# Optimization experiments

Measured on AMD Instinct MI355X. Metric: run time of the kernel, lower is better.

The kernel has to match this reference:

```python
import jax, jax.numpy as jnp
import numpy as np

B, L, C = 2, 2048, 1024
H, HD = 16, 64
MAX_SCALE_MUL = float(np.log(100.0))
SCALE = 1.0  # attn_l2_norm=True -> scale is 1


def setup_inputs() -> dict:
    key = jax.random.key(0)
    ks = jax.random.split(key, 6)
    x = jax.random.normal(ks[0], (B, L, C), dtype=jnp.float32)
    attn_bias = jax.random.normal(ks[1], (1, 1, L, L), dtype=jnp.float32)
    w_qkv = jax.random.normal(ks[2], (3 * C, C), dtype=jnp.float32) * (1.0 / np.sqrt(C))
    q_bias = jnp.zeros((C,), dtype=jnp.float32)
    v_bias = jnp.zeros((C,), dtype=jnp.float32)
    scale_mul = jnp.full((1, H, 1, 1), np.log(4.0), dtype=jnp.float32)  # scale_mul_1H11
    w_proj = jax.random.normal(ks[3], (C, C), dtype=jnp.float32) * (1.0 / np.sqrt(C))
    b_proj = jnp.zeros((C,), dtype=jnp.float32)
    return {"x": x, "attn_bias": attn_bias, "w_qkv": w_qkv, "q_bias": q_bias,
            "v_bias": v_bias, "scale_mul": scale_mul, "w_proj": w_proj, "b_proj": b_proj}


def reference(x, attn_bias, w_qkv, q_bias, v_bias, scale_mul, w_proj, b_proj):
    # qkv projection with concatenated bias (q_bias, zeros, v_bias)
    bias = jnp.concatenate([q_bias, jnp.zeros_like(q_bias), v_bias])  # [3C]
    qkv = jnp.einsum('blc,dc->bld', x, w_qkv) + bias                  # [B,L,3C]
    qkv = qkv.reshape(B, L, 3, H, HD).transpose(2, 0, 3, 1, 4)        # [3,B,H,L,HD]
    q, k, v = qkv[0], qkv[1], qkv[2]
    # attn_l2_norm path: L2-normalize q,k; q scaled by exp(clamped scale_mul)
    sm = jnp.exp(jnp.minimum(scale_mul, MAX_SCALE_MUL))               # [1,H,1,1]
    q = q / jnp.linalg.norm(q, axis=-1, keepdims=True) * sm
    k = k / jnp.linalg.norm(k, axis=-1, keepdims=True)
    # slow_attn: scaled scores + bias, softmax, weighted sum
    attn = jnp.einsum('bhld,bhmd->bhlm', q * SCALE, k) + attn_bias    # [B,H,L,L]
    p = jax.nn.softmax(attn, axis=-1)
    oup = jnp.einsum('bhlm,bhmd->bhld', p, v)                         # [B,H,L,HD]
    oup = oup.transpose(0, 2, 1, 3).reshape(B, L, C)
    return jnp.einsum('blc,dc->bld', oup, w_proj) + b_proj
```

## Files before the change

kernel.cpp:

```cpp
#include <hip/hip_runtime.h>
#include <cstdint>
#include <cstddef>
#include <math.h>

typedef __attribute__((ext_vector_type(8))) __bf16 bf16x8;
typedef __attribute__((ext_vector_type(4))) __bf16 bf16x4;
typedef __attribute__((ext_vector_type(4))) float f32x4;

#define AS1 __attribute__((address_space(1)))
#define AS3 __attribute__((address_space(3)))

#define LOG2E 1.4426950408889634f

__device__ __forceinline__ void gld16(void* lds_uniform, const void* gaddr) {
  __builtin_amdgcn_global_load_lds((const AS1 unsigned int*)gaddr,
                                   (AS3 unsigned int*)lds_uniform, 16, 0, 0);
}

__global__ __launch_bounds__(256)
void prep_kernel(const float* __restrict__ x, const float* __restrict__ wqkv,
                 const float* __restrict__ wproj, const float* __restrict__ bias,
                 __bf16* __restrict__ xb, __bf16* __restrict__ wqkvb,
                 __bf16* __restrict__ wprojb, __bf16* __restrict__ btr) {
  __shared__ __bf16 T[32][264];
  const int b = blockIdx.x;
  const int tid = threadIdx.x;
  if (b < 8192) {
    const float* src; __bf16* dst; int off;
    if (b < 4096)      { src = x;     dst = xb;     off = b; }
    else if (b < 7168) { src = wqkv;  dst = wqkvb;  off = b - 4096; }
    else               { src = wproj; dst = wprojb; off = b - 7168; }
    const int i = (off * 256 + tid) * 4;
    const float4 v = *(const float4*)(src + i);
    bf16x4 o;
    o[0] = (__bf16)v.x; o[1] = (__bf16)v.y; o[2] = (__bf16)v.z; o[3] = (__bf16)v.w;
    *(bf16x4*)(dst + i) = o;
    return;
  }
  const int bb = b - 8192;
  const int rb = bb >> 3, cg = bb & 7;
  const float* src = bias + (size_t)(rb * 32) * 2048 + cg * 256;
#pragma unroll
  for (int i = 0; i < 8; ++i) {
    const int u = i * 256 + tid;
    const int r = u >> 6, c4 = (u & 63) * 4;
    const float4 v = *(const float4*)(src + (size_t)r * 2048 + c4);
    T[r][c4 + 0] = (__bf16)(v.x * LOG2E);
    T[r][c4 + 1] = (__bf16)(v.y * LOG2E);
    T[r][c4 + 2] = (__bf16)(v.z * LOG2E);
    T[r][c4 + 3] = (__bf16)(v.w * LOG2E);
  }
  __syncthreads();
  const int ktl = tid >> 6;
  const int lane = tid & 63, g = lane >> 4, c = lane & 15;
  __bf16 outv[32];
#pragma unroll
  for (int v = 0; v < 32; ++v) {
    const int mi = v >> 4, ni = (v >> 2) & 3, j = v & 3;
    outv[v] = T[mi * 16 + g * 4 + j][ktl * 64 + ni * 16 + c];
  }
  __bf16* dst = btr + ((size_t)(rb * 32 + cg * 4 + ktl) * 64 + lane) * 32;
#pragma unroll
  for (int i = 0; i < 4; ++i)
    *(bf16x8*)(dst + i * 8) = *(bf16x8*)(outv + i * 8);
}

__global__ __launch_bounds__(256, 2)
void gemm_qkv_kernel(const __bf16* __restrict__ A, const __bf16* __restrict__ B,
                     const float* __restrict__ q_bias, const float* __restrict__ v_bias,
                     const float* __restrict__ scale_mul,
                     __bf16* __restrict__ qb, __bf16* __restrict__ ktp, __bf16* __restrict__ vb) {
  __shared__ __attribute__((aligned(16))) __bf16 As[128 * 32];
  __shared__ __attribute__((aligned(16))) __bf16 Bs[128 * 32];
  const int tid = threadIdx.x;
  const int w = tid >> 6, lane = tid & 63;
  const int m0 = blockIdx.y * 128, n0 = blockIdx.x * 128;
  const int wm = (w >> 1) * 64, wn = (w & 1) * 64;
  const int c = lane & 15, g = lane >> 4;
  f32x4 acc[4][4];
#pragma unroll
  for (int i = 0; i < 4; ++i)
#pragma unroll
    for (int j = 0; j < 4; ++j) acc[i][j] = (f32x4)(0.0f);

  const int r_row = lane >> 2;
  const int r_col = (lane & 3) * 16;
  const char* Abase = (const char*)A + (size_t)m0 * 2048;
  const char* Bbase = (const char*)B + (size_t)n0 * 2048;

  for (int kt = 0; kt < 1024; kt += 32) {
#pragma unroll
    for (int s = 0; s < 2; ++s) {
      const int R = w * 2 + s;
      const int row = R * 16 + r_row;
      gld16((char*)As + R * 1024, Abase + (size_t)row * 2048 + kt * 2 + r_col);
      gld16((char*)Bs + R * 1024, Bbase + (size_t)row * 2048 + kt * 2 + r_col);
    }
    __syncthreads();
    bf16x8 af[4], bfr[4];
#pragma unroll
    for (int i = 0; i < 4; ++i) {
      af[i]  = *(const bf16x8*)((const char*)As + (wm + i * 16 + c) * 64 + g * 16);
      bfr[i] = *(const bf16x8*)((const char*)Bs + (wn + i * 16 + c) * 64 + g * 16);
    }
#pragma unroll
    for (int ni = 0; ni < 4; ++ni)
#pragma unroll
      for (int mi = 0; mi < 4; ++mi)
        acc[ni][mi] = __builtin_amdgcn_mfma_f32_16x16x32_bf16(bfr[ni], af[mi], acc[ni][mi], 0, 0, 0);
    __syncthreads();
  }

  const int nbase = n0 + wn;
  const int which = nbase >> 10;
  const int h = (nbase >> 6) & 15;
  float smh = 1.0f;
  if (which == 0) smh = __expf(fminf(scale_mul[h], 4.605170185988091f)) * LOG2E;
  float4 cb[4];
#pragma unroll
  for (int ni = 0; ni < 4; ++ni) {
    if (which == 0)      cb[ni] = *(const float4*)(q_bias + nbase + ni * 16 + 4 * g);
    else if (which == 2) cb[ni] = *(const float4*)(v_bias + nbase - 2048 + ni * 16 + 4 * g);
    else                 cb[ni] = make_float4(0.f, 0.f, 0.f, 0.f);
  }
  const int mrow0 = m0 + wm;
  const int b2 = mrow0 >> 11;
  const int lpos0 = mrow0 & 2047;
  __bf16* kt_tile = ktp + (size_t)(b2 * 16 + h) * 131072 + (size_t)(lpos0 >> 6) * 4096;
  __bf16* dst_qv = ((which == 0) ? qb : vb) + ((size_t)((b2 * 16 + h) * 2048 + lpos0)) * 64;

#pragma unroll
  for (int mi = 0; mi < 4; ++mi) {
    float v[4][4];
    float ss = 0.0f;
#pragma unroll
    for (int ni = 0; ni < 4; ++ni) {
      v[ni][0] = acc[ni][mi][0] + cb[ni].x;
      v[ni][1] = acc[ni][mi][1] + cb[ni].y;
      v[ni][2] = acc[ni][mi][2] + cb[ni].z;
      v[ni][3] = acc[ni][mi][3] + cb[ni].w;
#pragma unroll
      for (int j = 0; j < 4; ++j) ss += v[ni][j] * v[ni][j];
    }
    ss += __shfl_xor(ss, 16, 64);
    ss += __shfl_xor(ss, 32, 64);
    const float sc = (which == 2) ? 1.0f : (rsqrtf(ss) * smh);
    const int key = mi * 16 + c;
    if (which == 1) {
#pragma unroll
      for (int ni = 0; ni < 4; ++ni) {
        bf16x4 pk;
        pk[0] = (__bf16)(v[ni][0] * sc); pk[1] = (__bf16)(v[ni][1] * sc);
        pk[2] = (__bf16)(v[ni][2] * sc); pk[3] = (__bf16)(v[ni][3] * sc);
        *(bf16x4*)(kt_tile + (ni >> 1) * 2048 + key * 32 + (ni & 1) * 16 + 4 * g) = pk;
      }
    } else {
      __bf16* drow = dst_qv + (size_t)key * 64;
#pragma unroll
      for (int ni = 0; ni < 4; ++ni) {
        bf16x4 pk;
        pk[0] = (__bf16)(v[ni][0] * sc); pk[1] = (__bf16)(v[ni][1] * sc);
        pk[2] = (__bf16)(v[ni][2] * sc); pk[3] = (__bf16)(v[ni][3] * sc);
        *(bf16x4*)(drow + ni * 16 + 4 * g) = pk;
      }
    }
  }
}

__global__ __launch_bounds__(256)
void vtrans_kernel(const __bf16* __restrict__ vb, __bf16* __restrict__ vtp) {
  __shared__ __attribute__((aligned(16))) __bf16 Vs[4][64 * 64];
  const int w = threadIdx.x >> 6, lane = threadIdx.x & 63;
  const int idx = blockIdx.x * 4 + w;
  const int bh = idx >> 5, tile = idx & 31;
  const __bf16* src = vb + ((size_t)bh * 2048 + tile * 64) * 64;
#pragma unroll
  for (int s = 0; s < 8; ++s)
    gld16((char*)&Vs[w][0] + s * 1024, (const char*)src + s * 1024 + lane * 16);
  __syncthreads();
  __bf16* outb = vtp + (size_t)idx * 4096;
#pragma unroll
  for (int r = 0; r < 8; ++r) {
    const int o = r * 512 + lane * 8;
    const int hd = (o >> 5) & 63;
    const int sl0 = ((o >> 11) << 5) | (o & 31);
    bf16x8 pk;
#pragma unroll
    for (int i = 0; i < 8; ++i) {
      const int slot = sl0 + i;
      const int key = (slot & 3) * 16 + (slot >> 2);
      pk[i] = Vs[w][key * 64 + hd];
    }
    *(bf16x8*)(outb + o) = pk;
  }
}

#define STAGE(t, b) {                                                          \
  const char* _ks = kp + (size_t)(t) * 8192 + w * 1024 + sl16;                 \
  const char* _vs = vp + (size_t)(t) * 8192 + w * 1024 + sl16;                 \
  gld16(&Kb[b][w * 1024], _ks);                                                \
  gld16(&Vb[b][w * 1024], _vs);                                                \
}

#define COMPUTE(t, b) {                                                        \
  const char* _bb = bp + ((size_t)(t) * 64 + lane) * 64 + MI * 32;             \
  bf16x8 bA[2];                                                                \
  bA[0] = *(const bf16x8*)_bb;                                                 \
  bA[1] = *(const bf16x8*)(_bb + 16);                                          \
  bf16x8 kf[4][2];                                                             \
  _Pragma("unroll")                                                            \
  for (int ni = 0; ni < 4; ++ni)                                               \
    _Pragma("unroll")                                                          \
    for (int ks = 0; ks < 2; ++ks)                                             \
      kf[ni][ks] = *(const bf16x8*)(&Kb[b][0] + ks * 4096 + (ni * 16 + c) * 64 + gsw16); \
  f32x4 sacc[4];                                                               \
  __builtin_amdgcn_s_setprio(1);                                               \
  _Pragma("unroll")                                                            \
  for (int ni = 0; ni < 4; ++ni) {                                             \
    f32x4 s_ = __builtin_amdgcn_mfma_f32_16x16x32_bf16(qf[0], kf[ni][0], (f32x4)(0.0f), 0, 0, 0); \
    sacc[ni] = __builtin_amdgcn_mfma_f32_16x16x32_bf16(qf[1], kf[ni][1], s_, 0, 0, 0); \
  }                                                                            \
  __builtin_amdgcn_s_setprio(0);                                               \
  _Pragma("unroll")                                                            \
  for (int j = 0; j < 4; ++j) {                                                \
    const float p0 = __builtin_amdgcn_exp2f(sacc[0][j] + (float)bA[(0 + j) >> 3][(0 + j) & 7]);   \
    const float p1 = __builtin_amdgcn_exp2f(sacc[1][j] + (float)bA[(4 + j) >> 3][(4 + j) & 7]);   \
    const float p2 = __builtin_amdgcn_exp2f(sacc[2][j] + (float)bA[(8 + j) >> 3][(8 + j) & 7]);   \
    const float p3 = __builtin_amdgcn_exp2f(sacc[3][j] + (float)bA[(12 + j) >> 3][(12 + j) & 7]); \
    lsum[j] += (p0 + p1) + (p2 + p3);                                          \
    bf16x4 pk;                                                                 \
    pk[0] = (__bf16)p0; pk[1] = (__bf16)p1; pk[2] = (__bf16)p2; pk[3] = (__bf16)p3; \
    *(bf16x4*)&Ps[w][c >> 3][g * 4 + j][(c & 7) * 4] = pk;                     \
  }                                                                            \
  bf16x8 pf[2];                                                                \
  _Pragma("unroll")                                                            \
  for (int ks = 0; ks < 2; ++ks)                                               \
    pf[ks] = *(const bf16x8*)&Ps[w][ks][c][g * 8];                             \
  __builtin_amdgcn_s_setprio(1);                                               \
  _Pragma("unroll")                                                            \
  for (int ni = 0; ni < 4; ++ni) {                                             \
    const bf16x8 v0 = *(const bf16x8*)(&Vb[b][0] + ni * 1024 + c * 64 + gsw16);        \
    const bf16x8 v1 = *(const bf16x8*)(&Vb[b][0] + 4096 + ni * 1024 + c * 64 + gsw16); \
    oacc[ni] = __builtin_amdgcn_mfma_f32_16x16x32_bf16(pf[0], v0, oacc[ni], 0, 0, 0);  \
    oacc[ni] = __builtin_amdgcn_mfma_f32_16x16x32_bf16(pf[1], v1, oacc[ni], 0, 0, 0);  \
  }                                                                            \
  __builtin_amdgcn_s_setprio(0);                                               \
}

__global__ __launch_bounds__(512, 4)
void attn_kernel(const __bf16* __restrict__ qb, const __bf16* __restrict__ ktp,
                 const __bf16* __restrict__ vtp, const __bf16* __restrict__ btr,
                 __bf16* __restrict__ oupb) {
  __shared__ __attribute__((aligned(16))) char Kb[2][8192];
  __shared__ __attribute__((aligned(16))) char Vb[2][8192];
  __shared__ __attribute__((aligned(16))) __bf16 Ps[8][2][16][40];
  const int tid = threadIdx.x, w = tid >> 6, lane = tid & 63;
  const int c = lane & 15, g = lane >> 4;
  const int MI = w & 1;
  const int sl16 = (lane ^ ((lane >> 3) & 3)) * 16;
  const int gsw16 = (g ^ ((c >> 1) & 3)) * 16;
  const int idx = blockIdx.x;
  const int bh = idx & 31, rb = idx >> 5;
  const __bf16* qh = qb + (size_t)bh * (2048 * 64);
  const char* kp = (const char*)ktp + (size_t)bh * (32 * 8192);
  const char* vp = (const char*)vtp + (size_t)bh * (32 * 8192);
  const char* bp = (const char*)btr + (size_t)(rb * 4 + (w >> 1)) * 131072;
  const int q0 = rb * 128 + w * 16;
  const int b2 = bh >> 4, h = bh & 15;

  bf16x8 qf[2];
#pragma unroll
  for (int ks = 0; ks < 2; ++ks)
    qf[ks] = *(const bf16x8*)(qh + (size_t)(q0 + c) * 64 + ks * 32 + g * 8);

  f32x4 oacc[4];
  float lsum[4];
#pragma unroll
  for (int ni = 0; ni < 4; ++ni) oacc[ni] = (f32x4)(0.0f);
#pragma unroll
  for (int j = 0; j < 4; ++j) lsum[j] = 0.0f;

  STAGE(0, 0);
  __syncthreads();
#pragma unroll 1
  for (int tt = 0; tt < 32; tt += 2) {
    if (tt + 1 < 32) STAGE(tt + 1, 1);
    COMPUTE(tt, 0);
    __syncthreads();
    if (tt + 2 < 32) STAGE(tt + 2, 0);
    COMPUTE(tt + 1, 1);
    __syncthreads();
  }

#pragma unroll
  for (int j = 0; j < 4; ++j) {
    float l = lsum[j];
    l += __shfl_xor(l, 1, 64);
    l += __shfl_xor(l, 2, 64);
    l += __shfl_xor(l, 4, 64);
    l += __shfl_xor(l, 8, 64);
    const float inv = 1.0f / l;
    const int qrow = q0 + g * 4 + j;
    __bf16* orow = oupb + ((size_t)(b2 * 2048 + qrow) * 16 + h) * 64;
#pragma unroll
    for (int ni = 0; ni < 4; ++ni)
      orow[ni * 16 + c] = (__bf16)(oacc[ni][j] * inv);
  }
}

__global__ __launch_bounds__(256, 2)
void gemm_proj_kernel(const __bf16* __restrict__ A, const __bf16* __restrict__ B,
                      const float* __restrict__ b_proj, float* __restrict__ out) {
  __shared__ __attribute__((aligned(16))) __bf16 As[64 * 32];
  __shared__ __attribute__((aligned(16))) __bf16 Bs[128 * 32];
  const int tid = threadIdx.x;
  const int w = tid >> 6, lane = tid & 63;
  const int c = lane & 15, g = lane >> 4;
  const int m0 = blockIdx.y * 64, n0 = blockIdx.x * 128;
  const int wm = (w >> 1) * 32, wn = (w & 1) * 64;
  f32x4 acc[2][4];
#pragma unroll
  for (int i = 0; i < 2; ++i)
#pragma unroll
    for (int j = 0; j < 4; ++j) acc[i][j] = (f32x4)(0.0f);

  const int r_row = lane >> 2;
  const int r_col = (lane & 3) * 16;
  const char* Abase = (const char*)A + (size_t)m0 * 2048;
  const char* Bbase = (const char*)B + (size_t)n0 * 2048;

  for (int kt = 0; kt < 1024; kt += 32) {
    {
      const int row = w * 16 + r_row;
      gld16((char*)As + w * 1024, Abase + (size_t)row * 2048 + kt * 2 + r_col);
    }
#pragma unroll
    for (int s = 0; s < 2; ++s) {
      const int R = w * 2 + s;
      const int row = R * 16 + r_row;
      gld16((char*)Bs + R * 1024, Bbase + (size_t)row * 2048 + kt * 2 + r_col);
    }
    __syncthreads();
    bf16x8 af[2], bfr[4];
#pragma unroll
    for (int i = 0; i < 2; ++i)
      af[i] = *(const bf16x8*)((const char*)As + (wm + i * 16 + c) * 64 + g * 16);
#pragma unroll
    for (int i = 0; i < 4; ++i)
      bfr[i] = *(const bf16x8*)((const char*)Bs + (wn + i * 16 + c) * 64 + g * 16);
#pragma unroll
    for (int mi = 0; mi < 2; ++mi)
#pragma unroll
      for (int ni = 0; ni < 4; ++ni)
        acc[mi][ni] = __builtin_amdgcn_mfma_f32_16x16x32_bf16(af[mi], bfr[ni], acc[mi][ni], 0, 0, 0);
    __syncthreads();
  }

  float cbias[4];
#pragma unroll
  for (int ni = 0; ni < 4; ++ni) cbias[ni] = b_proj[n0 + wn + ni * 16 + c];
#pragma unroll
  for (int mi = 0; mi < 2; ++mi)
#pragma unroll
    for (int j = 0; j < 4; ++j) {
      const int m = m0 + wm + mi * 16 + g * 4 + j;
      float* orow = out + (size_t)m * 1024 + n0 + wn;
#pragma unroll
      for (int ni = 0; ni < 4; ++ni)
        orow[ni * 16 + c] = acc[mi][ni][j] + cbias[ni];
    }
}

extern "C" void kernel_launch(void* const* d_in, const int* in_sizes, int n_in,
                              void* d_out, int out_size, void* d_ws, size_t ws_size,
                              hipStream_t stream) {
  const float* x         = (const float*)d_in[0];
  const float* attn_bias = (const float*)d_in[1];
  const float* w_qkv     = (const float*)d_in[2];
  const float* q_bias    = (const float*)d_in[3];
  const float* v_bias    = (const float*)d_in[4];
  const float* scale_mul = (const float*)d_in[5];
  const float* w_proj    = (const float*)d_in[6];
  const float* b_proj    = (const float*)d_in[7];
  float* out = (float*)d_out;

  __bf16* xb     = (__bf16*)d_ws;
  __bf16* wqkvb  = xb + 4194304;
  __bf16* wprojb = wqkvb + 3145728;
  __bf16* qb     = wprojb + 1048576;
  __bf16* ktp    = qb + 4194304;
  __bf16* vtp    = ktp + 4194304;
  __bf16* btr    = vtp + 4194304;
  __bf16* vb     = btr + 4194304;
  __bf16* oupb   = xb;

  prep_kernel<<<8704, 256, 0, stream>>>(x, w_qkv, w_proj, attn_bias, xb, wqkvb, wprojb, btr);
  gemm_qkv_kernel<<<dim3(24, 32), 256, 0, stream>>>(xb, wqkvb, q_bias, v_bias, scale_mul,
                                                    qb, ktp, vb);
  vtrans_kernel<<<256, 256, 0, stream>>>(vb, vtp);
  attn_kernel<<<512, 512, 0, stream>>>(qb, ktp, vtp, btr, oupb);
  gemm_proj_kernel<<<dim3(8, 64), 256, 0, stream>>>(oupb, wprojb, b_proj, out);
}
```

Measured before the change: 218.1 us.

## Compute transposed scores and pass P to PV MFMA via permlane swaps, dropping LDS

Swaps the MFMA operand order so each lane holds scores for a single query row across keys. P values are packed with v_cvt_pk_bf16_f32 and rearranged into PV-operand layout with v_permlane32/16_swap, replacing the per-tile round-trip through the Ps shared buffer. The bias and V transposition layouts in the prep and vtrans kernels change to match, and row sums need a different cross-lane reduction at the end. The aim is to remove LDS writes and reads from the attention inner loop, which relies on gfx950-specific permlane instructions and on the lane layouts being exactly right.

```diff
diff --git a/kernel.cpp b/kernel.cpp
--- a/kernel.cpp
+++ b/kernel.cpp
@@ -6,6 +6,7 @@
 typedef __attribute__((ext_vector_type(8))) __bf16 bf16x8;
 typedef __attribute__((ext_vector_type(4))) __bf16 bf16x4;
 typedef __attribute__((ext_vector_type(4))) float f32x4;
+typedef __attribute__((ext_vector_type(4))) unsigned int u32x4;
 
 #define AS1 __attribute__((address_space(1)))
 #define AS3 __attribute__((address_space(3)))
@@ -52,17 +53,19 @@
   }
   __syncthreads();
   const int ktl = tid >> 6;
-  const int lane = tid & 63, g = lane >> 4, c = lane & 15;
-  __bf16 outv[32];
-#pragma unroll
-  for (int v = 0; v < 32; ++v) {
-    const int mi = v >> 4, ni = (v >> 2) & 3, j = v & 3;
-    outv[v] = T[mi * 16 + g * 4 + j][ktl * 64 + ni * 16 + c];
-  }
-  __bf16* dst = btr + ((size_t)(rb * 32 + cg * 4 + ktl) * 64 + lane) * 32;
-#pragma unroll
-  for (int i = 0; i < 4; ++i)
-    *(bf16x8*)(dst + i * 8) = *(bf16x8*)(outv + i * 8);
+  const int lane = tid & 63, g = lane >> 4, cc = lane & 15;
+#pragma unroll
+  for (int sub = 0; sub < 2; ++sub) {
+    __bf16 outv[16];
+#pragma unroll
+    for (int v = 0; v < 16; ++v) {
+      const int ni = v >> 2, j = v & 3;
+      outv[v] = T[sub * 16 + cc][ktl * 64 + ni * 16 + g * 4 + j];
+    }
+    __bf16* dst = btr + ((size_t)(((rb * 2 + sub) * 32) + cg * 4 + ktl) * 64 + lane) * 16;
+    *(bf16x8*)(dst) = *(bf16x8*)(outv);
+    *(bf16x8*)(dst + 8) = *(bf16x8*)(outv + 8);
+  }
 }
 
 __global__ __launch_bounds__(256, 2)
@@ -179,18 +182,17 @@
     gld16((char*)&Vs[w][0] + s * 1024, (const char*)src + s * 1024 + lane * 16);
   __syncthreads();
   __bf16* outb = vtp + (size_t)idx * 4096;
+  const int gg = lane & 3, cc = lane >> 2;
 #pragma unroll
   for (int r = 0; r < 8; ++r) {
     const int o = r * 512 + lane * 8;
-    const int hd = (o >> 5) & 63;
-    const int sl0 = ((o >> 11) << 5) | (o & 31);
+    const int ni = r & 3, ks = r >> 2;
+    const int hd = ni * 16 + cc;
+    const int key0 = ks * 32 + gg * 8;
     bf16x8 pk;
 #pragma unroll
-    for (int i = 0; i < 8; ++i) {
-      const int slot = sl0 + i;
-      const int key = (slot & 3) * 16 + (slot >> 2);
-      pk[i] = Vs[w][key * 64 + hd];
-    }
+    for (int i = 0; i < 8; ++i)
+      pk[i] = Vs[w][(key0 + i) * 64 + hd];
     *(bf16x8*)(outb + o) = pk;
   }
 }
@@ -202,11 +204,12 @@
   gld16(&Vb[b][w * 1024], _vs);                                                \
 }
 
+#define BAV(ni, j) ((ni * 4 + j < 8) ? bA0[(ni * 4 + j) & 7] : bA1[(ni * 4 + j) & 7])
+
 #define COMPUTE(t, b) {                                                        \
-  const char* _bb = bp + ((size_t)(t) * 64 + lane) * 64 + MI * 32;             \
-  bf16x8 bA[2];                                                                \
-  bA[0] = *(const bf16x8*)_bb;                                                 \
-  bA[1] = *(const bf16x8*)(_bb + 16);                                          \
+  const char* _bb = bp + (size_t)(t) * 2048 + lane * 32;                       \
+  bf16x8 bA0 = *(const bf16x8*)_bb;                                            \
+  bf16x8 bA1 = *(const bf16x8*)(_bb + 16);                                     \
   bf16x8 kf[4][2];                                                             \
   _Pragma("unroll")                                                            \
   for (int ni = 0; ni < 4; ++ni)                                               \
@@ -217,32 +220,40 @@
   __builtin_amdgcn_s_setprio(1);                                               \
   _Pragma("unroll")                                                            \
   for (int ni = 0; ni < 4; ++ni) {                                             \
-    f32x4 s_ = __builtin_amdgcn_mfma_f32_16x16x32_bf16(qf[0], kf[ni][0], (f32x4)(0.0f), 0, 0, 0); \
-    sacc[ni] = __builtin_amdgcn_mfma_f32_16x16x32_bf16(qf[1], kf[ni][1], s_, 0, 0, 0); \
+    f32x4 s_ = __builtin_amdgcn_mfma_f32_16x16x32_bf16(kf[ni][0], qf[0], (f32x4)(0.0f), 0, 0, 0); \
+    sacc[ni] = __builtin_amdgcn_mfma_f32_16x16x32_bf16(kf[ni][1], qf[1], s_, 0, 0, 0); \
   }                                                                            \
   __builtin_amdgcn_s_setprio(0);                                               \
+  unsigned qp[4][2];                                                           \
   _Pragma("unroll")                                                            \
-  for (int j = 0; j < 4; ++j) {                                                \
-    const float p0 = __builtin_amdgcn_exp2f(sacc[0][j] + (float)bA[(0 + j) >> 3][(0 + j) & 7]);   \
-    const float p1 = __builtin_amdgcn_exp2f(sacc[1][j] + (float)bA[(4 + j) >> 3][(4 + j) & 7]);   \
-    const float p2 = __builtin_amdgcn_exp2f(sacc[2][j] + (float)bA[(8 + j) >> 3][(8 + j) & 7]);   \
-    const float p3 = __builtin_amdgcn_exp2f(sacc[3][j] + (float)bA[(12 + j) >> 3][(12 + j) & 7]); \
-    lsum[j] += (p0 + p1) + (p2 + p3);                                          \
-    bf16x4 pk;                                                                 \
-    pk[0] = (__bf16)p0; pk[1] = (__bf16)p1; pk[2] = (__bf16)p2; pk[3] = (__bf16)p3; \
-    *(bf16x4*)&Ps[w][c >> 3][g * 4 + j][(c & 7) * 4] = pk;                     \
+  for (int ni = 0; ni < 4; ++ni) {                                             \
+    const float p0 = __builtin_amdgcn_exp2f(sacc[ni][0] + (float)BAV(ni, 0));  \
+    const float p1 = __builtin_amdgcn_exp2f(sacc[ni][1] + (float)BAV(ni, 1));  \
+    const float p2 = __builtin_amdgcn_exp2f(sacc[ni][2] + (float)BAV(ni, 2));  \
+    const float p3 = __builtin_amdgcn_exp2f(sacc[ni][3] + (float)BAV(ni, 3));  \
+    lsum += (p0 + p1) + (p2 + p3);                                             \
+    asm("v_cvt_pk_bf16_f32 %0, %1, %2" : "=v"(qp[ni][0]) : "v"(p0), "v"(p1));  \
+    asm("v_cvt_pk_bf16_f32 %0, %1, %2" : "=v"(qp[ni][1]) : "v"(p2), "v"(p3));  \
   }                                                                            \
   bf16x8 pf[2];                                                                \
   _Pragma("unroll")                                                            \
-  for (int ks = 0; ks < 2; ++ks)                                               \
-    pf[ks] = *(const bf16x8*)&Ps[w][ks][c][g * 8];                             \
+  for (int ks = 0; ks < 2; ++ks) {                                             \
+    unsigned x0 = qp[2 * ks][0], x1 = qp[2 * ks][1];                           \
+    unsigned y0 = qp[2 * ks + 1][0], y1 = qp[2 * ks + 1][1];                   \
+    asm("v_permlane32_swap_b32 %0, %1" : "+v"(x0), "+v"(y0));                  \
+    asm("v_permlane16_swap_b32 %0, %1" : "+v"(x0), "+v"(y0));                  \
+    asm("v_permlane32_swap_b32 %0, %1" : "+v"(x1), "+v"(y1));                  \
+    asm("v_permlane16_swap_b32 %0, %1" : "+v"(x1), "+v"(y1));                  \
+    u32x4 t_; t_[0] = x0; t_[1] = x1; t_[2] = y0; t_[3] = y1;                  \
+    pf[ks] = __builtin_bit_cast(bf16x8, t_);                                   \
+  }                                                                            \
   __builtin_amdgcn_s_setprio(1);                                               \
   _Pragma("unroll")                                                            \
   for (int ni = 0; ni < 4; ++ni) {                                             \
-    const bf16x8 v0 = *(const bf16x8*)(&Vb[b][0] + ni * 1024 + c * 64 + gsw16);        \
-    const bf16x8 v1 = *(const bf16x8*)(&Vb[b][0] + 4096 + ni * 1024 + c * 64 + gsw16); \
-    oacc[ni] = __builtin_amdgcn_mfma_f32_16x16x32_bf16(pf[0], v0, oacc[ni], 0, 0, 0);  \
-    oacc[ni] = __builtin_amdgcn_mfma_f32_16x16x32_bf16(pf[1], v1, oacc[ni], 0, 0, 0);  \
+    const bf16x8 v0 = *(const bf16x8*)(&Vb[b][0] + 0 * 4096 + ni * 1024 + c * 64 + gsw16); \
+    const bf16x8 v1 = *(const bf16x8*)(&Vb[b][0] + 1 * 4096 + ni * 1024 + c * 64 + gsw16); \
+    oacc[ni] = __builtin_amdgcn_mfma_f32_16x16x32_bf16(pf[0], v0, oacc[ni], 0, 0, 0); \
+    oacc[ni] = __builtin_amdgcn_mfma_f32_16x16x32_bf16(pf[1], v1, oacc[ni], 0, 0, 0); \
   }                                                                            \
   __builtin_amdgcn_s_setprio(0);                                               \
 }
@@ -253,10 +264,8 @@
                  __bf16* __restrict__ oupb) {
   __shared__ __attribute__((aligned(16))) char Kb[2][8192];
   __shared__ __attribute__((aligned(16))) char Vb[2][8192];
-  __shared__ __attribute__((aligned(16))) __bf16 Ps[8][2][16][40];
   const int tid = threadIdx.x, w = tid >> 6, lane = tid & 63;
   const int c = lane & 15, g = lane >> 4;
-  const int MI = w & 1;
   const int sl16 = (lane ^ ((lane >> 3) & 3)) * 16;
   const int gsw16 = (g ^ ((c >> 1) & 3)) * 16;
   const int idx = blockIdx.x;
@@ -264,7 +273,7 @@
   const __bf16* qh = qb + (size_t)bh * (2048 * 64);
   const char* kp = (const char*)ktp + (size_t)bh * (32 * 8192);
   const char* vp = (const char*)vtp + (size_t)bh * (32 * 8192);
-  const char* bp = (const char*)btr + (size_t)(rb * 4 + (w >> 1)) * 131072;
+  const char* bp = (const char*)btr + (size_t)(rb * 8 + w) * 65536;
   const int q0 = rb * 128 + w * 16;
   const int b2 = bh >> 4, h = bh & 15;
 
@@ -274,11 +283,9 @@
     qf[ks] = *(const bf16x8*)(qh + (size_t)(q0 + c) * 64 + ks * 32 + g * 8);
 
   f32x4 oacc[4];
-  float lsum[4];
+  float lsum = 0.0f;
 #pragma unroll
   for (int ni = 0; ni < 4; ++ni) oacc[ni] = (f32x4)(0.0f);
-#pragma unroll
-  for (int j = 0; j < 4; ++j) lsum[j] = 0.0f;
 
   STAGE(0, 0);
   __syncthreads();
@@ -292,14 +299,13 @@
     __syncthreads();
   }
 
+  float l = lsum;
+  l += __shfl_xor(l, 16, 64);
+  l += __shfl_xor(l, 32, 64);
 #pragma unroll
   for (int j = 0; j < 4; ++j) {
-    float l = lsum[j];
-    l += __shfl_xor(l, 1, 64);
-    l += __shfl_xor(l, 2, 64);
-    l += __shfl_xor(l, 4, 64);
-    l += __shfl_xor(l, 8, 64);
-    const float inv = 1.0f / l;
+    const float lr = __shfl(l, g * 4 + j, 64);
+    const float inv = 1.0f / lr;
     const int qrow = q0 + g * 4 + j;
     __bf16* orow = oupb + ((size_t)(b2 * 2048 + qrow) * 16 + h) * 64;
 #pragma unroll
```

Result: no change. 216.2 us (-0.9%).
